# Kernel optimization log

Hardware: AMD Instinct MI355X
Metric: run time of the kernel (lower is better)

## Reference

```python
import jax, jax.numpy as jnp
import numpy as np

N = 32            # batch (age.shape[0])
N_SAMPLE = 8
S = N * N_SAMPLE  # posterior samples
T = 1024          # len_param
K = 64            # len_window
D = 4             # dim_target
P = 8             # dim_param
LOG2PI = float(np.log(2.0 * np.pi))


def _windows(x, axis, num, size):
    # torch.unfold equivalent, but window axis inserted right after `axis`
    idx = jnp.arange(num)[:, None] + jnp.arange(size)[None, :]
    return jnp.take(x, idx, axis=axis)


def _coeffs(a_pad):
    # a_pad: (2K-2, D, 1) -> AR weight matrix d: (K, K, D)
    # d[t, k] = prod(a[t-K+1+k+1 .. t]) with trailing 1 (reversed cumprod of windows)
    b = _windows(a_pad, 0, K, K - 1)                              # (K, K-1, D, 1)
    c = jnp.flip(jnp.cumprod(jnp.flip(b, 1), axis=1), 1)
    d = jnp.concatenate([c, jnp.ones_like(c[:, :1])], axis=1)      # (K, K, D, 1)
    return d[..., 0]                                               # (K, K, D)


def _window_param(z, d):
    # z: (S, K, D, P); d: (K, K, D) -> param: (S, K, D, P)
    z_pad = jnp.pad(z, ((0, 0), (K - 1, 0), (0, 0), (0, 0)))
    zwin = _windows(z_pad, 1, K, K)                                # (S, K, K, D, P)
    return jnp.einsum('stkdp,tkd->stdp', zwin, d)


def _forward(m, s_raw, a_raw, noise, dim_idx):
    mm = m[:, dim_idx]                         # (T, D, P)
    s = jax.nn.softplus(s_raw[:, dim_idx])     # scale_transform
    a = jax.nn.sigmoid(a_raw[:, dim_idx])      # (T-1, D, 1)
    # ---- first window ----
    a_pad = jnp.pad(a[:K - 1], ((K - 1, 0), (0, 0), (0, 0)))       # (2K-2, D, 1)
    mean = (1.0 - a_pad[K - 2:]) * mm[:K]                          # (K, D, P)
    sw = s[:K]
    z = mean + sw * noise[:, :K]                                   # rsample
    lp = -jnp.log(sw) - 0.5 * LOG2PI - 0.5 * ((z - mean) / sw) ** 2
    param = _window_param(z, _coeffs(a_pad))
    params, lps = [param], [lp]
    # ---- subsequent windows (sequential carry via param[:, -1]) ----
    for l in range(K, T, K):
        r = min(l + K, T)
        aw = a[l - 1:r - 1]                                        # (K, D, 1)
        mean = (1.0 - aw) * mm[l:r]
        sw = s[l:r]
        z = mean + sw * noise[:, l:r]
        lp = -jnp.log(sw) - 0.5 * LOG2PI - 0.5 * ((z - mean) / sw) ** 2
        a_pad = jnp.pad(aw[1:], ((K - 1, 0), (0, 0), (0, 0)))
        p = _window_param(z, _coeffs(a_pad))
        p = p + jnp.cumprod(aw, axis=0)[None] * param[:, -1][:, None]
        params.append(p)
        lps.append(lp)
        param = p
    return jnp.concatenate(params, axis=1), jnp.concatenate(lps, axis=1)


def setup_inputs() -> dict:
    key = jax.random.key(0)
    k = jax.random.split(key, 6)
    return {
        'y': jax.random.normal(k[0], (1, T, D), dtype=jnp.float32),
        'age': jax.random.uniform(k[1], (N,), dtype=jnp.float32),
        'm': 0.1 * jax.random.normal(k[2], (T, D, P), dtype=jnp.float32),
        's_raw': 0.1 * jax.random.normal(k[3], (T, D, P), dtype=jnp.float32) - 6.0,
        'a_raw': jax.random.normal(k[4], (T - 1, D, 1), dtype=jnp.float32),
        'noise': jax.random.normal(k[5], (S, T, D, P), dtype=jnp.float32),
        'cond_sample': jnp.zeros((S, D, P), dtype=jnp.float32),
        'dim_idx': jnp.arange(D, dtype=jnp.int32),
        'compute_log_prob': 1,
    }


def reference(y, age, m, s_raw, a_raw, noise, cond_sample, dim_idx, compute_log_prob):
    param, log_prob = _forward(m, s_raw, a_raw, noise, dim_idx)
    if compute_log_prob:
        return (param, log_prob)
    return param
```

## Files before the change

### kernel.cpp

```cpp
#include <hip/hip_runtime.h>

#define T_DIM 1024
#define D_DIM 4
#define P_DIM 8
#define S_DIM 256
#define DP 32
#define TDP (T_DIM * DP)
#define LOG2PI_F 1.8378770664093453f

__global__ __launch_bounds__(256) void build_tbl(
    const float* __restrict__ m,
    const float* __restrict__ s_raw,
    const float* __restrict__ a_raw,
    const int* __restrict__ dim_idx,
    float* __restrict__ tbl)
{
    int idx = blockIdx.x * 256 + threadIdx.x;
    int t = idx >> 5, dp = idx & 31, d = dp >> 3, p = dp & 7;
    int di = dim_idx[d];

    float mm = m[(t * D_DIM + di) * P_DIM + p];
    float sr = s_raw[(t * D_DIM + di) * P_DIM + p];
    float sv = (sr > 20.0f) ? sr : log1pf(expf(sr));
    float A = 0.0f;
    if (t > 0) A = 1.0f / (1.0f + expf(-a_raw[(t - 1) * D_DIM + di]));

    tbl[idx]           = (1.0f - A) * mm;
    tbl[TDP + idx]     = sv;
    tbl[2 * TDP + idx] = -logf(sv) - 0.5f * LOG2PI_F;
    tbl[3 * TDP + idx] = A;
}

__global__ __launch_bounds__(1024) void scan_kernel(
    const float* __restrict__ noise,
    const float* __restrict__ tbl,
    float* __restrict__ param_out,
    float* __restrict__ lp_out)
{
    const int tid  = threadIdx.x;
    const int qc   = tid & 7;
    const int cj   = tid >> 3;
    const int cjw  = cj & 7;
    const int wg   = tid >> 6;

    __shared__ float wtp[16][32];
    __shared__ float wtm[16][32];
    __shared__ float wci[16][32];

    const size_t sbase = (size_t)blockIdx.x * TDP;
    const int    off0  = cj * 8 * DP + qc * 4;

    float4 pl[8], Mk[8];
    float4 rp = make_float4(0.f, 0.f, 0.f, 0.f);
    float4 rm = make_float4(1.f, 1.f, 1.f, 1.f);
#pragma unroll
    for (int k = 0; k < 8; ++k) {
        const int o = off0 + k * DP;
        const float4 n  = *(const float4*)(noise + sbase + o);
        const float4 me = *(const float4*)(tbl + o);
        const float4 sv = *(const float4*)(tbl + TDP + o);
        const float4 nl = *(const float4*)(tbl + 2 * TDP + o);
        const float4 Aa = *(const float4*)(tbl + 3 * TDP + o);

        float4 lp;
        lp.x = nl.x - 0.5f * n.x * n.x;
        lp.y = nl.y - 0.5f * n.y * n.y;
        lp.z = nl.z - 0.5f * n.z * n.z;
        lp.w = nl.w - 0.5f * n.w * n.w;
        *(float4*)(lp_out + sbase + o) = lp;

        float4 z;
        z.x = me.x + sv.x * n.x;
        z.y = me.y + sv.y * n.y;
        z.z = me.z + sv.z * n.z;
        z.w = me.w + sv.w * n.w;

        rp.x = z.x + Aa.x * rp.x;  rm.x *= Aa.x;
        rp.y = z.y + Aa.y * rp.y;  rm.y *= Aa.y;
        rp.z = z.z + Aa.z * rp.z;  rm.z *= Aa.z;
        rp.w = z.w + Aa.w * rp.w;  rm.w *= Aa.w;
        pl[k] = rp;
        Mk[k] = rm;
    }

#pragma unroll
    for (int off = 1; off < 8; off <<= 1) {
        const int d = off * 8;
        float4 pp, pm;
        pp.x = __shfl_up(rp.x, d, 64);  pm.x = __shfl_up(rm.x, d, 64);
        pp.y = __shfl_up(rp.y, d, 64);  pm.y = __shfl_up(rm.y, d, 64);
        pp.z = __shfl_up(rp.z, d, 64);  pm.z = __shfl_up(rm.z, d, 64);
        pp.w = __shfl_up(rp.w, d, 64);  pm.w = __shfl_up(rm.w, d, 64);
        if (cjw >= off) {
            rp.x += rm.x * pp.x;  rm.x *= pm.x;
            rp.y += rm.y * pp.y;  rm.y *= pm.y;
            rp.z += rm.z * pp.z;  rm.z *= pm.z;
            rp.w += rm.w * pp.w;  rm.w *= pm.w;
        }
    }

    if (cjw == 7) {
        *(float4*)&wtp[wg][qc * 4] = rp;
        *(float4*)&wtm[wg][qc * 4] = rm;
    }
    __syncthreads();
    if (tid < 32) {
        float c = 0.0f;
#pragma unroll
        for (int g = 0; g < 16; ++g) {
            wci[g][tid] = c;
            c = wtp[g][tid] + wtm[g][tid] * c;
        }
    }
    __syncthreads();

    float4 ep, em;
    ep.x = __shfl_up(rp.x, 8, 64);  em.x = __shfl_up(rm.x, 8, 64);
    ep.y = __shfl_up(rp.y, 8, 64);  em.y = __shfl_up(rm.y, 8, 64);
    ep.z = __shfl_up(rp.z, 8, 64);  em.z = __shfl_up(rm.z, 8, 64);
    ep.w = __shfl_up(rp.w, 8, 64);  em.w = __shfl_up(rm.w, 8, 64);
    if (cjw == 0) {
        ep = make_float4(0.f, 0.f, 0.f, 0.f);
        em = make_float4(1.f, 1.f, 1.f, 1.f);
    }
    const float4 ci = *(const float4*)&wci[wg][qc * 4];
    float4 carry;
    carry.x = ep.x + em.x * ci.x;
    carry.y = ep.y + em.y * ci.y;
    carry.z = ep.z + em.z * ci.z;
    carry.w = ep.w + em.w * ci.w;

#pragma unroll
    for (int k = 0; k < 8; ++k) {
        const int o = off0 + k * DP;
        float4 pv;
        pv.x = pl[k].x + Mk[k].x * carry.x;
        pv.y = pl[k].y + Mk[k].y * carry.y;
        pv.z = pl[k].z + Mk[k].z * carry.z;
        pv.w = pl[k].w + Mk[k].w * carry.w;
        *(float4*)(param_out + sbase + o) = pv;
    }
}

extern "C" void kernel_launch(void* const* d_in, const int* in_sizes, int n_in,
                              void* d_out, int out_size, void* d_ws, size_t ws_size,
                              hipStream_t stream)
{
    const float* m      = (const float*)d_in[2];
    const float* s_raw  = (const float*)d_in[3];
    const float* a_raw  = (const float*)d_in[4];
    const float* noise  = (const float*)d_in[5];
    const int*   dimidx = (const int*)d_in[7];

    float* tbl = (float*)d_ws;

    float* param_out = (float*)d_out;
    float* lp_out    = param_out + (size_t)S_DIM * TDP;

    build_tbl<<<TDP / 256, 256, 0, stream>>>(m, s_raw, a_raw, dimidx, tbl);
    scan_kernel<<<S_DIM, 1024, 0, stream>>>(noise, tbl, param_out, lp_out);
}
```

Baseline: 129.7 us.

## Fuse table build into scan kernel and use nontemporal loads/stores

```diff
diff --git a/kernel.cpp b/kernel.cpp
--- a/kernel.cpp
+++ b/kernel.cpp
@@ -8,40 +8,26 @@
 #define TDP (T_DIM * DP)
 #define LOG2PI_F 1.8378770664093453f
 
-__global__ __launch_bounds__(256) void build_tbl(
+typedef float vf4 __attribute__((ext_vector_type(4)));
+
+__global__ __launch_bounds__(1024) void fused_scan(
+    const float* __restrict__ noise,
     const float* __restrict__ m,
     const float* __restrict__ s_raw,
     const float* __restrict__ a_raw,
     const int* __restrict__ dim_idx,
-    float* __restrict__ tbl)
-{
-    int idx = blockIdx.x * 256 + threadIdx.x;
-    int t = idx >> 5, dp = idx & 31, d = dp >> 3, p = dp & 7;
-    int di = dim_idx[d];
-
-    float mm = m[(t * D_DIM + di) * P_DIM + p];
-    float sr = s_raw[(t * D_DIM + di) * P_DIM + p];
-    float sv = (sr > 20.0f) ? sr : log1pf(expf(sr));
-    float A = 0.0f;
-    if (t > 0) A = 1.0f / (1.0f + expf(-a_raw[(t - 1) * D_DIM + di]));
-
-    tbl[idx]           = (1.0f - A) * mm;
-    tbl[TDP + idx]     = sv;
-    tbl[2 * TDP + idx] = -logf(sv) - 0.5f * LOG2PI_F;
-    tbl[3 * TDP + idx] = A;
-}
-
-__global__ __launch_bounds__(1024) void scan_kernel(
-    const float* __restrict__ noise,
-    const float* __restrict__ tbl,
     float* __restrict__ param_out,
     float* __restrict__ lp_out)
 {
-    const int tid  = threadIdx.x;
-    const int qc   = tid & 7;
-    const int cj   = tid >> 3;
-    const int cjw  = cj & 7;
-    const int wg   = tid >> 6;
+    const int tid = threadIdx.x;
+    const int qc  = tid & 7;
+    const int cj  = tid >> 3;
+    const int cjw = cj & 7;
+    const int wg  = tid >> 6;
+
+    const int d  = qc >> 1;
+    const int p0 = (qc & 1) * 4;
+    const int di = dim_idx[d];
 
     __shared__ float wtp[16][32];
     __shared__ float wtm[16][32];
@@ -50,47 +36,56 @@
     const size_t sbase = (size_t)blockIdx.x * TDP;
     const int    off0  = cj * 8 * DP + qc * 4;
 
-    float4 pl[8], Mk[8];
-    float4 rp = make_float4(0.f, 0.f, 0.f, 0.f);
-    float4 rm = make_float4(1.f, 1.f, 1.f, 1.f);
+    vf4 pl[8], Mk[8];
+    vf4 rp = (vf4){0.f, 0.f, 0.f, 0.f};
+    vf4 rm = (vf4){1.f, 1.f, 1.f, 1.f};
 #pragma unroll
     for (int k = 0; k < 8; ++k) {
+        const int t = cj * 8 + k;
         const int o = off0 + k * DP;
-        const float4 n  = *(const float4*)(noise + sbase + o);
-        const float4 me = *(const float4*)(tbl + o);
-        const float4 sv = *(const float4*)(tbl + TDP + o);
-        const float4 nl = *(const float4*)(tbl + 2 * TDP + o);
-        const float4 Aa = *(const float4*)(tbl + 3 * TDP + o);
+        const vf4 n  = __builtin_nontemporal_load((const vf4*)(noise + sbase + o));
+        const vf4 mv = *(const vf4*)(m     + (t * D_DIM + di) * P_DIM + p0);
+        const vf4 sr = *(const vf4*)(s_raw + (t * D_DIM + di) * P_DIM + p0);
 
-        float4 lp;
+        float A = 0.0f;
+        if (t > 0) A = 1.0f / (1.0f + __expf(-a_raw[(t - 1) * D_DIM + di]));
+        const float oma = 1.0f - A;
+
+        vf4 sv, nl;
+        sv.x = __logf(1.0f + __expf(sr.x));  nl.x = -__logf(sv.x) - 0.5f * LOG2PI_F;
+        sv.y = __logf(1.0f + __expf(sr.y));  nl.y = -__logf(sv.y) - 0.5f * LOG2PI_F;
+        sv.z = __logf(1.0f + __expf(sr.z));  nl.z = -__logf(sv.z) - 0.5f * LOG2PI_F;
+        sv.w = __logf(1.0f + __expf(sr.w));  nl.w = -__logf(sv.w) - 0.5f * LOG2PI_F;
+
+        vf4 lp;
         lp.x = nl.x - 0.5f * n.x * n.x;
         lp.y = nl.y - 0.5f * n.y * n.y;
         lp.z = nl.z - 0.5f * n.z * n.z;
         lp.w = nl.w - 0.5f * n.w * n.w;
-        *(float4*)(lp_out + sbase + o) = lp;
+        __builtin_nontemporal_store(lp, (vf4*)(lp_out + sbase + o));
 
-        float4 z;
-        z.x = me.x + sv.x * n.x;
-        z.y = me.y + sv.y * n.y;
-        z.z = me.z + sv.z * n.z;
-        z.w = me.w + sv.w * n.w;
+        vf4 z;
+        z.x = oma * mv.x + sv.x * n.x;
+        z.y = oma * mv.y + sv.y * n.y;
+        z.z = oma * mv.z + sv.z * n.z;
+        z.w = oma * mv.w + sv.w * n.w;
 
-        rp.x = z.x + Aa.x * rp.x;  rm.x *= Aa.x;
-        rp.y = z.y + Aa.y * rp.y;  rm.y *= Aa.y;
-        rp.z = z.z + Aa.z * rp.z;  rm.z *= Aa.z;
-        rp.w = z.w + Aa.w * rp.w;  rm.w *= Aa.w;
+        rp.x = z.x + A * rp.x;  rm.x *= A;
+        rp.y = z.y + A * rp.y;  rm.y *= A;
+        rp.z = z.z + A * rp.z;  rm.z *= A;
+        rp.w = z.w + A * rp.w;  rm.w *= A;
         pl[k] = rp;
         Mk[k] = rm;
     }
 
 #pragma unroll
     for (int off = 1; off < 8; off <<= 1) {
-        const int d = off * 8;
-        float4 pp, pm;
-        pp.x = __shfl_up(rp.x, d, 64);  pm.x = __shfl_up(rm.x, d, 64);
-        pp.y = __shfl_up(rp.y, d, 64);  pm.y = __shfl_up(rm.y, d, 64);
-        pp.z = __shfl_up(rp.z, d, 64);  pm.z = __shfl_up(rm.z, d, 64);
-        pp.w = __shfl_up(rp.w, d, 64);  pm.w = __shfl_up(rm.w, d, 64);
+        const int dd = off * 8;
+        vf4 pp, pm;
+        pp.x = __shfl_up(rp.x, dd, 64);  pm.x = __shfl_up(rm.x, dd, 64);
+        pp.y = __shfl_up(rp.y, dd, 64);  pm.y = __shfl_up(rm.y, dd, 64);
+        pp.z = __shfl_up(rp.z, dd, 64);  pm.z = __shfl_up(rm.z, dd, 64);
+        pp.w = __shfl_up(rp.w, dd, 64);  pm.w = __shfl_up(rm.w, dd, 64);
         if (cjw >= off) {
             rp.x += rm.x * pp.x;  rm.x *= pm.x;
             rp.y += rm.y * pp.y;  rm.y *= pm.y;
@@ -100,8 +95,8 @@
     }
 
     if (cjw == 7) {
-        *(float4*)&wtp[wg][qc * 4] = rp;
-        *(float4*)&wtm[wg][qc * 4] = rm;
+        *(vf4*)&wtp[wg][qc * 4] = rp;
+        *(vf4*)&wtm[wg][qc * 4] = rm;
     }
     __syncthreads();
     if (tid < 32) {
@@ -114,17 +109,17 @@
     }
     __syncthreads();
 
-    float4 ep, em;
+    vf4 ep, em;
     ep.x = __shfl_up(rp.x, 8, 64);  em.x = __shfl_up(rm.x, 8, 64);
     ep.y = __shfl_up(rp.y, 8, 64);  em.y = __shfl_up(rm.y, 8, 64);
     ep.z = __shfl_up(rp.z, 8, 64);  em.z = __shfl_up(rm.z, 8, 64);
     ep.w = __shfl_up(rp.w, 8, 64);  em.w = __shfl_up(rm.w, 8, 64);
     if (cjw == 0) {
-        ep = make_float4(0.f, 0.f, 0.f, 0.f);
-        em = make_float4(1.f, 1.f, 1.f, 1.f);
+        ep = (vf4){0.f, 0.f, 0.f, 0.f};
+        em = (vf4){1.f, 1.f, 1.f, 1.f};
     }
-    const float4 ci = *(const float4*)&wci[wg][qc * 4];
-    float4 carry;
+    const vf4 ci = *(const vf4*)&wci[wg][qc * 4];
+    vf4 carry;
     carry.x = ep.x + em.x * ci.x;
     carry.y = ep.y + em.y * ci.y;
     carry.z = ep.z + em.z * ci.z;
@@ -133,12 +128,12 @@
 #pragma unroll
     for (int k = 0; k < 8; ++k) {
         const int o = off0 + k * DP;
-        float4 pv;
+        vf4 pv;
         pv.x = pl[k].x + Mk[k].x * carry.x;
         pv.y = pl[k].y + Mk[k].y * carry.y;
         pv.z = pl[k].z + Mk[k].z * carry.z;
         pv.w = pl[k].w + Mk[k].w * carry.w;
-        *(float4*)(param_out + sbase + o) = pv;
+        __builtin_nontemporal_store(pv, (vf4*)(param_out + sbase + o));
     }
 }
 
@@ -152,11 +147,9 @@
     const float* noise  = (const float*)d_in[5];
     const int*   dimidx = (const int*)d_in[7];
 
-    float* tbl = (float*)d_ws;
-
     float* param_out = (float*)d_out;
     float* lp_out    = param_out + (size_t)S_DIM * TDP;
 
-    build_tbl<<<TDP / 256, 256, 0, stream>>>(m, s_raw, a_raw, dimidx, tbl);
-    scan_kernel<<<S_DIM, 1024, 0, stream>>>(noise, tbl, param_out, lp_out);
+    fused_scan<<<S_DIM, 1024, 0, stream>>>(noise, m, s_raw, a_raw, dimidx,
+                                           param_out, lp_out);
 }
```

New measurement: 119.2 us. 8.1% less time.
